# Kernel tuning notes

Hardware: AMD Instinct MI355X
Metric: run time of the kernel (lower is better)

The kernel has to match this reference:

```python
import jax, jax.numpy as jnp
import numpy as np

WAVELET_LEN = 64
N_SCALES = 8
MIN_SCALE, MAX_SCALE = 1.0, 32.0
SPARSITY_THRESHOLD = 1e-4


def _morlet_bank():
    # matches AdaptiveWaveletTransform._initialize_mother_wavelets
    t = jnp.linspace(-4.0, 4.0, WAVELET_LEN)
    i = jnp.arange(N_SCALES, dtype=jnp.float32)
    omega = 2.0 + i * 0.5           # [n_scales]
    sigma = 1.0 + i * 0.1
    w = jnp.exp(-t[None, :] ** 2 / (2.0 * sigma[:, None] ** 2)) * jnp.cos(omega[:, None] * t[None, :])
    return w / jnp.linalg.norm(w, axis=1, keepdims=True)  # [n_scales, 64]


def setup_inputs() -> dict:
    key = jax.random.key(0)
    signal = jax.random.normal(key, (16, 4096, 64), dtype=jnp.float32)
    mother_wavelets = _morlet_bank().astype(jnp.float32)   # learned param
    scale_weights = jnp.ones((N_SCALES,), dtype=jnp.float32)  # learned param
    return {"signal": signal, "mother_wavelets": mother_wavelets, "scale_weights": scale_weights}


def reference(signal, mother_wavelets, scale_weights):
    # scales are static (registered buffer) -> compute in numpy
    scales = np.logspace(np.log10(MIN_SCALE), np.log10(MAX_SCALE), N_SCALES)
    B, S, F = signal.shape
    per_scale = []
    grid = jnp.arange(WAVELET_LEN, dtype=jnp.float32)
    for idx in range(N_SCALES):
        scale = float(scales[idx])
        L = int(WAVELET_LEN * scale)  # dilated kernel length (static)
        # F.interpolate(mode='linear', align_corners=True): sample at linspace(0, 63, L)
        xq = jnp.linspace(0.0, WAVELET_LEN - 1.0, L)
        kern = jnp.interp(xq, grid, mother_wavelets[idx]) / np.sqrt(scale)  # [L]
        n = S + L - 1                      # full conv length
        n_fft = 1 << int(np.ceil(np.log2(n)))  # next pow2 (static)
        # vectorized FFT conv over batch and features simultaneously
        sig_f = jnp.fft.rfft(signal, n=n_fft, axis=1)      # [B, n_fft//2+1, F]
        k_f = jnp.fft.rfft(kern, n=n_fft)                   # [n_fft//2+1]
        conv = jnp.fft.irfft(sig_f * k_f[None, :, None], n=n_fft, axis=1)
        per_scale.append(conv[:, :S, :])   # L>=64 so n>=S always
    coeffs = jnp.stack(per_scale, axis=1)  # [B, n_scales, S, F]
    coeffs = coeffs * scale_weights[None, :, None, None]
    # use_sparse + eval-mode thresholding
    mask = (jnp.abs(coeffs) > SPARSITY_THRESHOLD).astype(coeffs.dtype)
    return coeffs * mask
```

## Files before the change

kernel.cpp:

```cpp
#include <hip/hip_runtime.h>
#include <hip/hip_bf16.h>
#include <math.h>

#define S_LEN 4096
#define N_FEAT 64
#define N_BATCH 16
#define N_SCALES 8
#define THRESH 1e-4f
#define PADL 2048
#define NCHUNK ((PADL + S_LEN) / 16)
#define CHUNK_ELEMS 1024

typedef unsigned short ushort_t;
typedef __attribute__((ext_vector_type(8))) short bf16x8;
typedef __attribute__((ext_vector_type(16))) float f32x16;

struct ScaleParams {
    int L[N_SCALES], Lpad[N_SCALES], off[N_SCALES];
    int Mc[N_SCALES], Aoff[N_SCALES];
    float inv_sqrt_scale[N_SCALES], step[N_SCALES];
};

__global__ void build_kernels(const float* __restrict__ mother,
                              float* __restrict__ kern,
                              ScaleParams p, int total) {
    int i = blockIdx.x * blockDim.x + threadIdx.x;
    if (i >= total) return;
    int idx = 0;
#pragma unroll
    for (int s = 1; s < N_SCALES; ++s)
        if (i >= p.off[s]) idx = s;
    int l = i - p.off[idx];
    float v = 0.f;
    if (l < p.L[idx]) {
        float xq = fminf(l * p.step[idx], 63.0f);
        int i0 = (int)xq; if (i0 > 62) i0 = 62;
        float frac = xq - (float)i0;
        float a = mother[idx * 64 + i0];
        float b = mother[idx * 64 + i0 + 1];
        v = (a + (b - a) * frac) * p.inv_sqrt_scale[idx];
    }
    kern[i] = v;
}

__global__ void prep_A(const float* __restrict__ kern, ushort_t* __restrict__ Atab,
                       ScaleParams p, int totalA) {
    int i = blockIdx.x * blockDim.x + threadIdx.x;
    if (i >= totalA) return;
    int idx = 0;
#pragma unroll
    for (int s = 1; s < N_SCALES; ++s)
        if (i >= p.Aoff[s]) idx = s;
    int rel = i - p.Aoff[idx];
    int m = rel >> 9;
    int r = rel & 511;
    int lane = r >> 3, e = r & 7;
    int ti = lane & 31, sj = 8 * (lane >> 5) + e;
    int kidx = 16 * m - 16 + ti - sj;
    float v = (kidx >= 0 && kidx < p.Lpad[idx]) ? kern[p.off[idx] + kidx] : 0.f;
    __hip_bfloat16 hh = __float2bfloat16(v);
    Atab[i] = *reinterpret_cast<ushort_t*>(&hh);
}

__global__ __launch_bounds__(256) void transpose_sig(const float* __restrict__ sig,
                                                     ushort_t* __restrict__ XTc) {
    const int b = blockIdx.y;
    const int G = blockIdx.x * 4 + (threadIdx.x >> 6);
    const int l = threadIdx.x & 63;
    unsigned int u[4];
    if (G < PADL / 8) {
        u[0] = u[1] = u[2] = u[3] = 0u;
    } else {
        const float* sp = sig + ((size_t)b * S_LEN + ((size_t)G * 8 - PADL)) * N_FEAT + l;
#pragma unroll
        for (int j = 0; j < 4; ++j) {
            float v0 = sp[(size_t)(2 * j) * N_FEAT];
            float v1 = sp[(size_t)(2 * j + 1) * N_FEAT];
            __hip_bfloat16 h0 = __float2bfloat16(v0);
            __hip_bfloat16 h1 = __float2bfloat16(v1);
            u[j] = (unsigned int)*reinterpret_cast<ushort_t*>(&h0) |
                   ((unsigned int)*reinterpret_cast<ushort_t*>(&h1) << 16);
        }
    }
    uint4 vv = {u[0], u[1], u[2], u[3]};
    *reinterpret_cast<uint4*>(XTc + (size_t)b * (NCHUNK * CHUNK_ELEMS)
                              + (size_t)G * 512 + l * 8) = vv;
}

__global__ __launch_bounds__(256) void wavelet_mfma(
    const ushort_t* __restrict__ XTc, const ushort_t* __restrict__ Atab,
    const float* __restrict__ sw, float* __restrict__ out, ScaleParams p) {
    const int idx = 7 - blockIdx.z;
    const int b = blockIdx.y;
    const int wave = threadIdx.x >> 6, lane = threadIdx.x & 63;
    const int tw0 = blockIdx.x * 256 + wave * 64;
    const int h = lane >> 5, fc = lane & 31;
    const int Mc = p.Mc[idx];

    const ushort_t* Ab = Atab + p.Aoff[idx] + lane * 8;
    const int c0 = (PADL + tw0) / 16 + 1;
    const ushort_t* Bp = XTc + (size_t)b * (NCHUNK * CHUNK_ELEMS)
                       + (size_t)(c0 * 2 + h) * 512 + fc * 8;

    f32x16 a00, a01, a10, a11;
#pragma unroll
    for (int r = 0; r < 16; ++r) { a00[r] = 0.f; a01[r] = 0.f; a10[r] = 0.f; a11[r] = 0.f; }

#pragma unroll
    for (int mm = -2; mm < 0; ++mm) {
        const ushort_t* q = Bp + (size_t)(-mm) * 1024;
        bf16x8 A1p = *reinterpret_cast<const bf16x8*>(Ab + (mm + 2) * 512);
        bf16x8 X0p = *reinterpret_cast<const bf16x8*>(q);
        bf16x8 X1p = *reinterpret_cast<const bf16x8*>(q + 256);
        a10 = __builtin_amdgcn_mfma_f32_32x32x16_bf16(A1p, X0p, a10, 0, 0, 0);
        a11 = __builtin_amdgcn_mfma_f32_32x32x16_bf16(A1p, X1p, a11, 0, 0, 0);
    }

    bf16x8 A0 = *reinterpret_cast<const bf16x8*>(Ab);
    bf16x8 A1 = *reinterpret_cast<const bf16x8*>(Ab + 1024);
    bf16x8 X0 = *reinterpret_cast<const bf16x8*>(Bp);
    bf16x8 X1 = *reinterpret_cast<const bf16x8*>(Bp + 256);

#pragma unroll 2
    for (int mm = 0; mm < Mc; ++mm) {
        const int mn = mm + 1;
        const int mnc = (mn < Mc) ? mn : (Mc - 1);
        const ushort_t* qa = Ab + (size_t)mn * 512;
        const ushort_t* qb = Bp - (size_t)mnc * 1024;
        bf16x8 nA0 = *reinterpret_cast<const bf16x8*>(qa);
        bf16x8 nA1 = *reinterpret_cast<const bf16x8*>(qa + 1024);
        bf16x8 nX0 = *reinterpret_cast<const bf16x8*>(qb);
        bf16x8 nX1 = *reinterpret_cast<const bf16x8*>(qb + 256);
        a00 = __builtin_amdgcn_mfma_f32_32x32x16_bf16(A0, X0, a00, 0, 0, 0);
        a01 = __builtin_amdgcn_mfma_f32_32x32x16_bf16(A0, X1, a01, 0, 0, 0);
        a10 = __builtin_amdgcn_mfma_f32_32x32x16_bf16(A1, X0, a10, 0, 0, 0);
        a11 = __builtin_amdgcn_mfma_f32_32x32x16_bf16(A1, X1, a11, 0, 0, 0);
        A0 = nA0; A1 = nA1; X0 = nX0; X1 = nX1;
    }

    const float w = sw[idx];
    float* ob = out + ((size_t)(b * N_SCALES + idx) * S_LEN + tw0) * N_FEAT + fc;
#pragma unroll
    for (int r = 0; r < 16; ++r) {
        const int row = (r & 3) + 8 * (r >> 2) + 4 * h;
        float v;
        v = a00[r] * w; v = (fabsf(v) > THRESH) ? v : 0.f;
        __builtin_nontemporal_store(v, &ob[(size_t)row * N_FEAT]);
        v = a01[r] * w; v = (fabsf(v) > THRESH) ? v : 0.f;
        __builtin_nontemporal_store(v, &ob[(size_t)row * N_FEAT + 32]);
        v = a10[r] * w; v = (fabsf(v) > THRESH) ? v : 0.f;
        __builtin_nontemporal_store(v, &ob[(size_t)(row + 32) * N_FEAT]);
        v = a11[r] * w; v = (fabsf(v) > THRESH) ? v : 0.f;
        __builtin_nontemporal_store(v, &ob[(size_t)(row + 32) * N_FEAT + 32]);
    }
}

extern "C" void kernel_launch(void* const* d_in, const int* in_sizes, int n_in,
                              void* d_out, int out_size, void* d_ws, size_t ws_size,
                              hipStream_t stream) {
    const float* sig    = (const float*)d_in[0];
    const float* mother = (const float*)d_in[1];
    const float* sw     = (const float*)d_in[2];
    float* out = (float*)d_out;

    float*    kern = (float*)d_ws;
    ushort_t* Atab = (ushort_t*)((char*)d_ws + 32768);
    ushort_t* XTc  = (ushort_t*)((char*)d_ws + 524288);

    ScaleParams p;
    int off = 0, aoff = 0;
    for (int i = 0; i < N_SCALES; ++i) {
        double scale = pow(10.0, (double)i * log10(32.0) / 7.0);
        double v = 64.0 * scale;
        double r = floor(v + 0.5);
        int L = (fabs(v - r) < 1e-6) ? (int)r : (int)v;
        p.L[i] = L;
        p.Lpad[i] = (L + 15) & ~15;
        p.off[i] = off;           off += p.Lpad[i];
        p.Mc[i] = (L + 46) >> 4;
        p.Aoff[i] = aoff;         aoff += (p.Mc[i] + 3) * 512;
        p.inv_sqrt_scale[i] = (float)(1.0 / sqrt(scale));
        p.step[i] = (float)(63.0 / (double)(L - 1));
    }
    const int totalK = off;
    const int totalA = aoff;

    build_kernels<<<dim3((totalK + 255) / 256), dim3(256), 0, stream>>>(
        mother, kern, p, totalK);
    prep_A<<<dim3((totalA + 255) / 256), dim3(256), 0, stream>>>(
        kern, Atab, p, totalA);
    transpose_sig<<<dim3((PADL + S_LEN) / 32, N_BATCH), dim3(256), 0, stream>>>(
        sig, XTc);

    wavelet_mfma<<<dim3(S_LEN / 256, N_BATCH, N_SCALES), dim3(256), 0, stream>>>(
        XTc, Atab, sw, out, p);
}
```

Baseline: 87.26 us.

## Widen per-wave output tile to 128 rows with rotating A register ring

Each wave now computes 128 time rows instead of 64, with eight accumulator tiles, and keeps a ring of eight Toeplitz A fragments in registers so each loaded signal chunk feeds eight MFMAs. The aim is to raise MFMA-to-load ratio and cut redundant A/X reloads. The kernel-building pass is also fused into prep_A, removing one launch. The cost is higher VGPR pressure (128 accumulator registers plus the ring), half as many blocks, and padded iteration counts that add some zero work.

```diff
diff --git a/kernel.cpp b/kernel.cpp
--- a/kernel.cpp
+++ b/kernel.cpp
@@ -9,41 +9,18 @@
 #define THRESH 1e-4f
 #define PADL 2048
 #define NCHUNK ((PADL + S_LEN) / 16)
-#define CHUNK_ELEMS 1024
+#define BCHUNK_ELEMS 1024
 
 typedef unsigned short ushort_t;
 typedef __attribute__((ext_vector_type(8))) short bf16x8;
 typedef __attribute__((ext_vector_type(16))) float f32x16;
 
 struct ScaleParams {
-    int L[N_SCALES], Lpad[N_SCALES], off[N_SCALES];
-    int Mc[N_SCALES], Aoff[N_SCALES];
+    int L[N_SCALES], Mc[N_SCALES], Niter[N_SCALES], Aoff[N_SCALES];
     float inv_sqrt_scale[N_SCALES], step[N_SCALES];
 };
 
-__global__ void build_kernels(const float* __restrict__ mother,
-                              float* __restrict__ kern,
-                              ScaleParams p, int total) {
-    int i = blockIdx.x * blockDim.x + threadIdx.x;
-    if (i >= total) return;
-    int idx = 0;
-#pragma unroll
-    for (int s = 1; s < N_SCALES; ++s)
-        if (i >= p.off[s]) idx = s;
-    int l = i - p.off[idx];
-    float v = 0.f;
-    if (l < p.L[idx]) {
-        float xq = fminf(l * p.step[idx], 63.0f);
-        int i0 = (int)xq; if (i0 > 62) i0 = 62;
-        float frac = xq - (float)i0;
-        float a = mother[idx * 64 + i0];
-        float b = mother[idx * 64 + i0 + 1];
-        v = (a + (b - a) * frac) * p.inv_sqrt_scale[idx];
-    }
-    kern[i] = v;
-}
-
-__global__ void prep_A(const float* __restrict__ kern, ushort_t* __restrict__ Atab,
+__global__ void prep_A(const float* __restrict__ mother, ushort_t* __restrict__ Atab,
                        ScaleParams p, int totalA) {
     int i = blockIdx.x * blockDim.x + threadIdx.x;
     if (i >= totalA) return;
@@ -52,12 +29,20 @@
     for (int s = 1; s < N_SCALES; ++s)
         if (i >= p.Aoff[s]) idx = s;
     int rel = i - p.Aoff[idx];
-    int m = rel >> 9;
+    int ci = rel >> 9;
     int r = rel & 511;
     int lane = r >> 3, e = r & 7;
     int ti = lane & 31, sj = 8 * (lane >> 5) + e;
-    int kidx = 16 * m - 16 + ti - sj;
-    float v = (kidx >= 0 && kidx < p.Lpad[idx]) ? kern[p.off[idx] + kidx] : 0.f;
+    int kidx = 16 * (ci - 6) - 16 + ti - sj;
+    float v = 0.f;
+    if (kidx >= 0 && kidx < p.L[idx]) {
+        float xq = fminf(kidx * p.step[idx], 63.0f);
+        int i0 = (int)xq; if (i0 > 62) i0 = 62;
+        float frac = xq - (float)i0;
+        float a = mother[idx * 64 + i0];
+        float b = mother[idx * 64 + i0 + 1];
+        v = (a + (b - a) * frac) * p.inv_sqrt_scale[idx];
+    }
     __hip_bfloat16 hh = __float2bfloat16(v);
     Atab[i] = *reinterpret_cast<ushort_t*>(&hh);
 }
@@ -83,9 +68,11 @@
         }
     }
     uint4 vv = {u[0], u[1], u[2], u[3]};
-    *reinterpret_cast<uint4*>(XTc + (size_t)b * (NCHUNK * CHUNK_ELEMS)
+    *reinterpret_cast<uint4*>(XTc + (size_t)b * (NCHUNK * BCHUNK_ELEMS)
                               + (size_t)G * 512 + l * 8) = vv;
 }
+
+#define MFMA(A, X, C) C = __builtin_amdgcn_mfma_f32_32x32x16_bf16(A, X, C, 0, 0, 0)
 
 __global__ __launch_bounds__(256) void wavelet_mfma(
     const ushort_t* __restrict__ XTc, const ushort_t* __restrict__ Atab,
@@ -93,66 +80,78 @@
     const int idx = 7 - blockIdx.z;
     const int b = blockIdx.y;
     const int wave = threadIdx.x >> 6, lane = threadIdx.x & 63;
-    const int tw0 = blockIdx.x * 256 + wave * 64;
+    const int tw0 = blockIdx.x * 512 + wave * 128;
     const int h = lane >> 5, fc = lane & 31;
-    const int Mc = p.Mc[idx];
+    const int niter = p.Niter[idx];
+    const int c0 = (PADL + tw0) / 16 + 1;
 
     const ushort_t* Ab = Atab + p.Aoff[idx] + lane * 8;
-    const int c0 = (PADL + tw0) / 16 + 1;
-    const ushort_t* Bp = XTc + (size_t)b * (NCHUNK * CHUNK_ELEMS)
-                       + (size_t)(c0 * 2 + h) * 512 + fc * 8;
+    const ushort_t* Bb = XTc + (size_t)b * (NCHUNK * BCHUNK_ELEMS)
+                       + h * 512 + fc * 8;
 
-    f32x16 a00, a01, a10, a11;
+    f32x16 c00, c01, c10, c11, c20, c21, c30, c31;
 #pragma unroll
-    for (int r = 0; r < 16; ++r) { a00[r] = 0.f; a01[r] = 0.f; a10[r] = 0.f; a11[r] = 0.f; }
-
-#pragma unroll
-    for (int mm = -2; mm < 0; ++mm) {
-        const ushort_t* q = Bp + (size_t)(-mm) * 1024;
-        bf16x8 A1p = *reinterpret_cast<const bf16x8*>(Ab + (mm + 2) * 512);
-        bf16x8 X0p = *reinterpret_cast<const bf16x8*>(q);
-        bf16x8 X1p = *reinterpret_cast<const bf16x8*>(q + 256);
-        a10 = __builtin_amdgcn_mfma_f32_32x32x16_bf16(A1p, X0p, a10, 0, 0, 0);
-        a11 = __builtin_amdgcn_mfma_f32_32x32x16_bf16(A1p, X1p, a11, 0, 0, 0);
+    for (int r = 0; r < 16; ++r) {
+        c00[r] = 0.f; c01[r] = 0.f; c10[r] = 0.f; c11[r] = 0.f;
+        c20[r] = 0.f; c21[r] = 0.f; c30[r] = 0.f; c31[r] = 0.f;
     }
 
-    bf16x8 A0 = *reinterpret_cast<const bf16x8*>(Ab);
-    bf16x8 A1 = *reinterpret_cast<const bf16x8*>(Ab + 1024);
-    bf16x8 X0 = *reinterpret_cast<const bf16x8*>(Bp);
-    bf16x8 X1 = *reinterpret_cast<const bf16x8*>(Bp + 256);
+    bf16x8 Ar[8];
+#pragma unroll
+    for (int i = 0; i < 8; ++i)
+        Ar[i] = *reinterpret_cast<const bf16x8*>(Ab + i * 512);
+    bf16x8 Xe0 = *reinterpret_cast<const bf16x8*>(Bb + (size_t)(c0 + 6) * 1024);
+    bf16x8 Xe1 = *reinterpret_cast<const bf16x8*>(Bb + (size_t)(c0 + 6) * 1024 + 256);
+    bf16x8 Xo0 = *reinterpret_cast<const bf16x8*>(Bb + (size_t)(c0 + 5) * 1024);
+    bf16x8 Xo1 = *reinterpret_cast<const bf16x8*>(Bb + (size_t)(c0 + 5) * 1024 + 256);
 
-#pragma unroll 2
-    for (int mm = 0; mm < Mc; ++mm) {
-        const int mn = mm + 1;
-        const int mnc = (mn < Mc) ? mn : (Mc - 1);
-        const ushort_t* qa = Ab + (size_t)mn * 512;
-        const ushort_t* qb = Bp - (size_t)mnc * 1024;
-        bf16x8 nA0 = *reinterpret_cast<const bf16x8*>(qa);
-        bf16x8 nA1 = *reinterpret_cast<const bf16x8*>(qa + 1024);
-        bf16x8 nX0 = *reinterpret_cast<const bf16x8*>(qb);
-        bf16x8 nX1 = *reinterpret_cast<const bf16x8*>(qb + 256);
-        a00 = __builtin_amdgcn_mfma_f32_32x32x16_bf16(A0, X0, a00, 0, 0, 0);
-        a01 = __builtin_amdgcn_mfma_f32_32x32x16_bf16(A0, X1, a01, 0, 0, 0);
-        a10 = __builtin_amdgcn_mfma_f32_32x32x16_bf16(A1, X0, a10, 0, 0, 0);
-        a11 = __builtin_amdgcn_mfma_f32_32x32x16_bf16(A1, X1, a11, 0, 0, 0);
-        A0 = nA0; A1 = nA1; X0 = nX0; X1 = nX1;
+    const ushort_t* Apf = Ab + 8 * 512;
+    const ushort_t* Bpf = Bb + (size_t)(c0 + 4) * 1024;
+
+    for (int it = 0; it < niter; it += 8) {
+#pragma unroll
+        for (int ph = 0; ph < 8; ++ph) {
+            bf16x8 a0 = Ar[ph & 7];
+            bf16x8 a1 = Ar[(ph + 2) & 7];
+            bf16x8 a2 = Ar[(ph + 4) & 7];
+            bf16x8 a3 = Ar[(ph + 6) & 7];
+            bf16x8 x0 = (ph & 1) ? Xo0 : Xe0;
+            bf16x8 x1 = (ph & 1) ? Xo1 : Xe1;
+            Ar[ph & 7] = *reinterpret_cast<const bf16x8*>(Apf);
+            Apf += 512;
+            if (ph & 1) {
+                Xo0 = *reinterpret_cast<const bf16x8*>(Bpf);
+                Xo1 = *reinterpret_cast<const bf16x8*>(Bpf + 256);
+            } else {
+                Xe0 = *reinterpret_cast<const bf16x8*>(Bpf);
+                Xe1 = *reinterpret_cast<const bf16x8*>(Bpf + 256);
+            }
+            Bpf -= 1024;
+            MFMA(a0, x0, c00); MFMA(a0, x1, c01);
+            MFMA(a1, x0, c10); MFMA(a1, x1, c11);
+            MFMA(a2, x0, c20); MFMA(a2, x1, c21);
+            MFMA(a3, x0, c30); MFMA(a3, x1, c31);
+        }
     }
 
     const float w = sw[idx];
     float* ob = out + ((size_t)(b * N_SCALES + idx) * S_LEN + tw0) * N_FEAT + fc;
-#pragma unroll
-    for (int r = 0; r < 16; ++r) {
-        const int row = (r & 3) + 8 * (r >> 2) + 4 * h;
-        float v;
-        v = a00[r] * w; v = (fabsf(v) > THRESH) ? v : 0.f;
-        __builtin_nontemporal_store(v, &ob[(size_t)row * N_FEAT]);
-        v = a01[r] * w; v = (fabsf(v) > THRESH) ? v : 0.f;
-        __builtin_nontemporal_store(v, &ob[(size_t)row * N_FEAT + 32]);
-        v = a10[r] * w; v = (fabsf(v) > THRESH) ? v : 0.f;
-        __builtin_nontemporal_store(v, &ob[(size_t)(row + 32) * N_FEAT]);
-        v = a11[r] * w; v = (fabsf(v) > THRESH) ? v : 0.f;
-        __builtin_nontemporal_store(v, &ob[(size_t)(row + 32) * N_FEAT + 32]);
+#define STORE_TILE(CLO, CHI, JT)                                               \
+    {                                                                          \
+        _Pragma("unroll") for (int r = 0; r < 16; ++r) {                       \
+            const int row = (JT) * 32 + (r & 3) + 8 * (r >> 2) + 4 * h;        \
+            float v;                                                           \
+            v = CLO[r] * w; v = (fabsf(v) > THRESH) ? v : 0.f;                 \
+            __builtin_nontemporal_store(v, &ob[(size_t)row * N_FEAT]);         \
+            v = CHI[r] * w; v = (fabsf(v) > THRESH) ? v : 0.f;                 \
+            __builtin_nontemporal_store(v, &ob[(size_t)row * N_FEAT + 32]);    \
+        }                                                                      \
     }
+    STORE_TILE(c00, c01, 0)
+    STORE_TILE(c10, c11, 1)
+    STORE_TILE(c20, c21, 2)
+    STORE_TILE(c30, c31, 3)
+#undef STORE_TILE
 }
 
 extern "C" void kernel_launch(void* const* d_in, const int* in_sizes, int n_in,
@@ -163,35 +162,31 @@
     const float* sw     = (const float*)d_in[2];
     float* out = (float*)d_out;
 
-    float*    kern = (float*)d_ws;
     ushort_t* Atab = (ushort_t*)((char*)d_ws + 32768);
     ushort_t* XTc  = (ushort_t*)((char*)d_ws + 524288);
 
     ScaleParams p;
-    int off = 0, aoff = 0;
+    int aoff = 0;
     for (int i = 0; i < N_SCALES; ++i) {
         double scale = pow(10.0, (double)i * log10(32.0) / 7.0);
         double v = 64.0 * scale;
         double r = floor(v + 0.5);
         int L = (fabs(v - r) < 1e-6) ? (int)r : (int)v;
         p.L[i] = L;
-        p.Lpad[i] = (L + 15) & ~15;
-        p.off[i] = off;           off += p.Lpad[i];
         p.Mc[i] = (L + 46) >> 4;
-        p.Aoff[i] = aoff;         aoff += (p.Mc[i] + 3) * 512;
+        p.Niter[i] = (p.Mc[i] + 13) & ~7;
+        p.Aoff[i] = aoff;
+        aoff += (p.Niter[i] + 8) * 512;
         p.inv_sqrt_scale[i] = (float)(1.0 / sqrt(scale));
         p.step[i] = (float)(63.0 / (double)(L - 1));
     }
-    const int totalK = off;
     const int totalA = aoff;
 
-    build_kernels<<<dim3((totalK + 255) / 256), dim3(256), 0, stream>>>(
-        mother, kern, p, totalK);
     prep_A<<<dim3((totalA + 255) / 256), dim3(256), 0, stream>>>(
-        kern, Atab, p, totalA);
+        mother, Atab, p, totalA);
     transpose_sig<<<dim3((PADL + S_LEN) / 32, N_BATCH), dim3(256), 0, stream>>>(
         sig, XTc);
 
-    wavelet_mfma<<<dim3(S_LEN / 256, N_BATCH, N_SCALES), dim3(256), 0, stream>>>(
+    wavelet_mfma<<<dim3(S_LEN / 512, N_BATCH, N_SCALES), dim3(256), 0, stream>>>(
         XTc, Atab, sw, out, p);
 }
```

Result: no change. 87.93 us (+0.8%).
